# Kernel tuning notes

Hardware: AMD Instinct MI355X
Metric: run time of the kernel (lower is better)

Reference implementation:

```python
import jax, jax.numpy as jnp
import numpy as np

ITERATIONS = 10
EPS = 1e-8
ALPHA = 1.0
BETA = 1.0


def _conv3x3x3(x):
    # all-ones 3x3x3 kernel, padding=1 (SAME), single channel; NCDHW layout
    k = jnp.ones((1, 1, 3, 3, 3), x.dtype)
    return jax.lax.conv_general_dilated(
        x, k, window_strides=(1, 1, 1), padding='SAME',
        dimension_numbers=('NCDHW', 'OIDHW', 'NCDHW'))


def _soft_skeletonize(x):
    x = jax.nn.sigmoid(x)
    skeleton = x
    for _ in range(ITERATIONS):
        eroded = (_conv3x3x3(skeleton) > 0).astype(x.dtype)
        opened = (_conv3x3x3(eroded) > 0).astype(x.dtype)
        skeleton = jnp.clip(skeleton - opened, 0.0, 1.0)
    return skeleton


def _count_components(binary):
    neighbors = _conv3x3x3(binary)
    mask = binary > 0
    cnt = jnp.sum(mask).astype(binary.dtype)
    # torch.mean(neighbors[mask] + eps) == sum((neighbors+eps)*mask)/cnt
    mean_nb = jnp.sum(jnp.where(mask, neighbors + EPS, 0.0)) / jnp.maximum(cnt, 1.0)
    return (cnt / mean_nb)[None]


def setup_inputs() -> dict:
    key = jax.random.key(0)
    k1, k2 = jax.random.split(key)
    pred = jax.random.normal(k1, (2, 1, 192, 192, 192), dtype=jnp.float32)
    target = jax.random.uniform(k2, (2, 1, 192, 192, 192), dtype=jnp.float32)
    return {"pred": pred, "target": target}


def reference(pred, target):
    pred_prob = jax.nn.sigmoid(pred)
    # NOTE: module applies sigmoid again inside _soft_skeletonize (faithful)
    pred_skeleton = _soft_skeletonize(pred_prob)
    target_skeleton = _soft_skeletonize(target)

    intersection = jnp.sum(pred_skeleton * target_skeleton)
    union = jnp.sum(pred_skeleton) + jnp.sum(target_skeleton)
    skeleton_loss = 1.0 - (2.0 * intersection + EPS) / (union + EPS)

    pred_binary = (pred_prob > 0.5).astype(pred.dtype)
    target_binary = target  # .float() no-op
    pred_components = _count_components(pred_binary)
    target_components = _count_components(target_binary)
    connectivity_loss = jnp.mean(jnp.abs(pred_components - target_components))

    return ALPHA * skeleton_loss + BETA * connectivity_loss
```

## Files before the change

### kernel.cpp

```cpp
#include <hip/hip_runtime.h>
#include <math.h>

#define NN 192
#define PLANE (NN * NN)
#define VOL (NN * NN * NN)
#define ZCHUNK 12
#define RP 96
#define NBIN 8
#define EPSF 1e-8f

template <int MODE>
__device__ __forceinline__ float bval(float u) {
  return (MODE == 0) ? ((u > 0.f) ? 1.f : 0.f) : u;
}

struct PlaneR {
  float4 a, b, c, d;
};

__device__ __forceinline__ void loadP(const float* __restrict__ base, int z,
                                      int offA, int offB, int offC, int offD,
                                      int xoff, PlaneR& P) {
  const int zz = min(max(z, 0), NN - 1);
  const float* p = base + (size_t)zz * PLANE;
  P.a = *(const float4*)(p + offA + xoff);
  P.b = *(const float4*)(p + offB + xoff);
  P.c = *(const float4*)(p + offC + xoff);
  P.d = *(const float4*)(p + offD + xoff);
}

template <int MODE>
__device__ __forceinline__ void consume2(const PlaneR& P, float mA, float mD, float mz,
                                         int lane, float4& sY, float4& sZ,
                                         float4& cY, float4& cZ) {
  const float a0 = bval<MODE>(P.a.x), a1 = bval<MODE>(P.a.y), a2 = bval<MODE>(P.a.z), a3 = bval<MODE>(P.a.w);
  const float b0 = bval<MODE>(P.b.x), b1 = bval<MODE>(P.b.y), b2 = bval<MODE>(P.b.z), b3 = bval<MODE>(P.b.w);
  const float c0 = bval<MODE>(P.c.x), c1 = bval<MODE>(P.c.y), c2 = bval<MODE>(P.c.z), c3 = bval<MODE>(P.c.w);
  const float d0 = bval<MODE>(P.d.x), d1 = bval<MODE>(P.d.y), d2 = bval<MODE>(P.d.z), d3 = bval<MODE>(P.d.w);
  const float u0 = b0 + c0, u1 = b1 + c1, u2 = b2 + c2, u3 = b3 + c3;
  const float tY0 = fmaf(a0, mA, u0), tY1 = fmaf(a1, mA, u1), tY2 = fmaf(a2, mA, u2), tY3 = fmaf(a3, mA, u3);
  const float tZ0 = fmaf(d0, mD, u0), tZ1 = fmaf(d1, mD, u1), tZ2 = fmaf(d2, mD, u2), tZ3 = fmaf(d3, mD, u3);
  const float upY = __shfl_up(tY3, 1), dnY = __shfl_down(tY0, 1);
  const float upZ = __shfl_up(tZ3, 1), dnZ = __shfl_down(tZ0, 1);
  const float tlY = (lane == 0) ? 0.f : upY;
  const float trY = (lane >= 47) ? 0.f : dnY;
  const float tlZ = (lane == 0) ? 0.f : upZ;
  const float trZ = (lane >= 47) ? 0.f : dnZ;
  const float pY01 = tY0 + tY1, pY23 = tY2 + tY3;
  const float pZ01 = tZ0 + tZ1, pZ23 = tZ2 + tZ3;
  sY.x = (tlY + pY01) * mz; sY.y = (pY01 + tY2) * mz; sY.z = (tY1 + pY23) * mz; sY.w = (pY23 + trY) * mz;
  sZ.x = (tlZ + pZ01) * mz; sZ.y = (pZ01 + tZ2) * mz; sZ.z = (tZ1 + pZ23) * mz; sZ.w = (pZ23 + trZ) * mz;
  cY.x = b0; cY.y = b1; cY.z = b2; cY.w = b3;
  cZ.x = c0; cZ.y = c1; cZ.z = c2; cZ.w = c3;
}

#define ACC1(C, SP, SC, SN)                                   \
  {                                                           \
    float m = ((C) > 0.f) ? act : 0.f;                        \
    cnt += m;                                                 \
    acc = fmaf(m, ((SP) + (SC)) + (SN), acc);                 \
  }

#define ACCUM8(snY, snZ)                      \
  ACC1(cY.x, spY.x, scY.x, (snY).x)           \
  ACC1(cY.y, spY.y, scY.y, (snY).y)           \
  ACC1(cY.z, spY.z, scY.z, (snY).z)           \
  ACC1(cY.w, spY.w, scY.w, (snY).w)           \
  ACC1(cZ.x, spZ.x, scZ.x, (snZ).x)           \
  ACC1(cZ.y, spZ.y, scZ.y, (snZ).y)           \
  ACC1(cZ.z, spZ.z, scZ.z, (snZ).z)           \
  ACC1(cZ.w, spZ.w, scZ.w, (snZ).w)

#define ROTATE(snY, snZ, cnY, cnZ) \
  spY = scY; scY = snY; spZ = scZ; scZ = snZ; cY = cnY; cZ = cnZ;

#define STEP_R(PSLOT, I)                                                   \
  {                                                                        \
    float4 snY, snZ, cnY, cnZ;                                             \
    consume2<MODE>(PSLOT, mA, mD, 1.f, lane, snY, snZ, cnY, cnZ);          \
    loadP(base, z0 + 4 + (I), offA, offB, offC, offD, xoff, PSLOT);        \
    ACCUM8(snY, snZ);                                                      \
    ROTATE(snY, snZ, cnY, cnZ);                                            \
  }

#define STEP_E(PSLOT, MZ)                                                  \
  {                                                                        \
    float4 snY, snZ, cnY, cnZ;                                             \
    consume2<MODE>(PSLOT, mA, mD, (MZ), lane, snY, snZ, cnY, cnZ);         \
    ACCUM8(snY, snZ);                                                      \
    ROTATE(snY, snZ, cnY, cnZ);                                            \
  }

template <int MODE>
__device__ __forceinline__ void unit2(const float* __restrict__ base, int y0, int z0,
                                      int xoff, float act, int lane,
                                      float& cnt, float& acc) {
  const int offB = y0 * NN;
  const int offA = (y0 > 0 ? y0 - 1 : 0) * NN;
  const int offC = (y0 + 1) * NN;
  const int offD = (y0 + 2 < NN ? y0 + 2 : NN - 1) * NN;
  const float mA = (y0 > 0) ? 1.f : 0.f;
  const float mD = (y0 + 2 < NN) ? 1.f : 0.f;
  const float mzLo = (z0 > 0) ? 1.f : 0.f;
  const float mzHi = (z0 + ZCHUNK < NN) ? 1.f : 0.f;

  PlaneR P0, P1, P2;
  loadP(base, z0 - 1, offA, offB, offC, offD, xoff, P0);
  loadP(base, z0,     offA, offB, offC, offD, xoff, P1);
  loadP(base, z0 + 1, offA, offB, offC, offD, xoff, P2);

  float4 spY, scY, spZ, scZ, cY, cZ, j1, j2;
  consume2<MODE>(P0, mA, mD, mzLo, lane, spY, spZ, j1, j2);
  loadP(base, z0 + 2, offA, offB, offC, offD, xoff, P0);
  consume2<MODE>(P1, mA, mD, 1.f, lane, scY, scZ, cY, cZ);
  loadP(base, z0 + 3, offA, offB, offC, offD, xoff, P1);

#pragma unroll 1
  for (int i = 0; i < 9; i += 3) {
    STEP_R(P2, i + 0);
    STEP_R(P0, i + 1);
    STEP_R(P1, i + 2);
  }
  STEP_E(P2, 1.f);
  STEP_E(P0, 1.f);
  STEP_E(P1, mzHi);
}

__global__ void init_ws(float* __restrict__ ws) {
  if (threadIdx.x < NBIN * 16) ws[threadIdx.x] = 0.f;
}

__global__ __launch_bounds__(64, 2) void skel_main(const float* __restrict__ pred,
                                                   const float* __restrict__ target,
                                                   float* __restrict__ ws) {
  const int b = blockIdx.x;
  const int xcd = b & 7;
  const int slot = b >> 3;
  const int g = slot / RP;
  const int yp = slot % RP;
  const int unit = xcd * 8 + g;
  const int vol = unit & 3;
  const int zc = unit >> 2;
  const int z0 = zc * ZCHUNK;
  const int y0 = 2 * yp;
  const float* base = (vol < 2 ? pred : target) + (size_t)(vol & 1) * VOL;

  const int lane = threadIdx.x;
  const int xoff = 4 * min(lane, 47);
  const float act = (lane < 48) ? 1.f : 0.f;

  float cnt = 0.f, acc = 0.f;
  if (vol < 2) unit2<0>(base, y0, z0, xoff, act, lane, cnt, acc);
  else         unit2<1>(base, y0, z0, xoff, act, lane, cnt, acc);

#pragma unroll
  for (int o = 32; o > 0; o >>= 1) {
    cnt += __shfl_down(cnt, o);
    acc += __shfl_down(acc, o);
  }
  if (lane == 0) {
    const int off = (vol < 2) ? 0 : 2;
    float* slot_p = &ws[((yp & (NBIN - 1)) << 4) + off];
    atomicAdd(slot_p + 0, cnt);
    atomicAdd(slot_p + 1, acc);
  }
}

__global__ void finalize(const float* __restrict__ ws, float* __restrict__ out) {
  if (threadIdx.x == 0 && blockIdx.x == 0) {
    float cp = 0.f, ap = 0.f, ct = 0.f, at = 0.f;
#pragma unroll
    for (int i = 0; i < NBIN; ++i) {
      cp += ws[i * 16 + 0];
      ap += ws[i * 16 + 1];
      ct += ws[i * 16 + 2];
      at += ws[i * 16 + 3];
    }
    float mp = (ap + EPSF * cp) / fmaxf(cp, 1.f);
    float Pc = cp / mp;
    float mt = (at + EPSF * ct) / fmaxf(ct, 1.f);
    float Tc = ct / mt;
    out[0] = fabsf(Pc - Tc);
  }
}

extern "C" void kernel_launch(void* const* d_in, const int* in_sizes, int n_in,
                              void* d_out, int out_size, void* d_ws, size_t ws_size,
                              hipStream_t stream) {
  const float* pred = (const float*)d_in[0];
  const float* target = (const float*)d_in[1];
  float* ws = (float*)d_ws;
  float* out = (float*)d_out;

  init_ws<<<1, 128, 0, stream>>>(ws);
  skel_main<<<dim3(6144), dim3(64), 0, stream>>>(pred, target, ws);
  finalize<<<1, 64, 0, stream>>>(ws, out);
}
```

Before: 149.5 us.

## Process two interleaved z-chunks per wavefront to raise memory-level parallelism

Each 64-thread block now handles two z-chunks (A and B) of the same y-pair and volume, interleaving their plane loads and stencil steps. This halves the grid to 3072 blocks and relaxes launch bounds to one block per SIMD, so more registers are available. The goal is more independent loads in flight per wave, hiding HBM latency. The cost is fewer waves overall and higher register pressure, which could reduce occupancy-driven latency hiding.

Measured after the change: 143.7 us. 3.9% less time.

```diff
diff --git a/kernel.cpp b/kernel.cpp
--- a/kernel.cpp
+++ b/kernel.cpp
@@ -61,87 +61,106 @@
     acc = fmaf(m, ((SP) + (SC)) + (SN), acc);                 \
   }
 
-#define ACCUM8(snY, snZ)                      \
-  ACC1(cY.x, spY.x, scY.x, (snY).x)           \
-  ACC1(cY.y, spY.y, scY.y, (snY).y)           \
-  ACC1(cY.z, spY.z, scY.z, (snY).z)           \
-  ACC1(cY.w, spY.w, scY.w, (snY).w)           \
-  ACC1(cZ.x, spZ.x, scZ.x, (snZ).x)           \
-  ACC1(cZ.y, spZ.y, scZ.y, (snZ).y)           \
-  ACC1(cZ.z, spZ.z, scZ.z, (snZ).z)           \
-  ACC1(cZ.w, spZ.w, scZ.w, (snZ).w)
-
-#define ROTATE(snY, snZ, cnY, cnZ) \
-  spY = scY; scY = snY; spZ = scZ; scZ = snZ; cY = cnY; cZ = cnZ;
-
-#define STEP_R(PSLOT, I)                                                   \
+#define ACCUM8(S, snY, snZ)                            \
+  ACC1(cY##S.x, spY##S.x, scY##S.x, (snY).x)           \
+  ACC1(cY##S.y, spY##S.y, scY##S.y, (snY).y)           \
+  ACC1(cY##S.z, spY##S.z, scY##S.z, (snY).z)           \
+  ACC1(cY##S.w, spY##S.w, scY##S.w, (snY).w)           \
+  ACC1(cZ##S.x, spZ##S.x, scZ##S.x, (snZ).x)           \
+  ACC1(cZ##S.y, spZ##S.y, scZ##S.y, (snZ).y)           \
+  ACC1(cZ##S.z, spZ##S.z, scZ##S.z, (snZ).z)           \
+  ACC1(cZ##S.w, spZ##S.w, scZ##S.w, (snZ).w)
+
+#define ROT(S, snY, snZ, cnY, cnZ)                                        \
+  spY##S = scY##S; scY##S = snY; spZ##S = scZ##S; scZ##S = snZ;           \
+  cY##S = cnY; cZ##S = cnZ;
+
+#define STEP_R(S, PSLOT, Z0, I)                                            \
   {                                                                        \
     float4 snY, snZ, cnY, cnZ;                                             \
     consume2<MODE>(PSLOT, mA, mD, 1.f, lane, snY, snZ, cnY, cnZ);          \
-    loadP(base, z0 + 4 + (I), offA, offB, offC, offD, xoff, PSLOT);        \
-    ACCUM8(snY, snZ);                                                      \
-    ROTATE(snY, snZ, cnY, cnZ);                                            \
-  }
-
-#define STEP_E(PSLOT, MZ)                                                  \
+    loadP(base, (Z0) + 4 + (I), offA, offB, offC, offD, xoff, PSLOT);      \
+    ACCUM8(S, snY, snZ);                                                   \
+    ROT(S, snY, snZ, cnY, cnZ);                                            \
+  }
+
+#define STEP_E(S, PSLOT, MZ)                                               \
   {                                                                        \
     float4 snY, snZ, cnY, cnZ;                                             \
     consume2<MODE>(PSLOT, mA, mD, (MZ), lane, snY, snZ, cnY, cnZ);         \
-    ACCUM8(snY, snZ);                                                      \
-    ROTATE(snY, snZ, cnY, cnZ);                                            \
+    ACCUM8(S, snY, snZ);                                                   \
+    ROT(S, snY, snZ, cnY, cnZ);                                            \
   }
 
 template <int MODE>
-__device__ __forceinline__ void unit2(const float* __restrict__ base, int y0, int z0,
-                                      int xoff, float act, int lane,
-                                      float& cnt, float& acc) {
+__device__ __forceinline__ void unit2x2(const float* __restrict__ base, int y0,
+                                        int z0A, int z0B, int xoff, float act,
+                                        int lane, float& cnt, float& acc) {
   const int offB = y0 * NN;
   const int offA = (y0 > 0 ? y0 - 1 : 0) * NN;
   const int offC = (y0 + 1) * NN;
   const int offD = (y0 + 2 < NN ? y0 + 2 : NN - 1) * NN;
   const float mA = (y0 > 0) ? 1.f : 0.f;
   const float mD = (y0 + 2 < NN) ? 1.f : 0.f;
-  const float mzLo = (z0 > 0) ? 1.f : 0.f;
-  const float mzHi = (z0 + ZCHUNK < NN) ? 1.f : 0.f;
-
-  PlaneR P0, P1, P2;
-  loadP(base, z0 - 1, offA, offB, offC, offD, xoff, P0);
-  loadP(base, z0,     offA, offB, offC, offD, xoff, P1);
-  loadP(base, z0 + 1, offA, offB, offC, offD, xoff, P2);
-
-  float4 spY, scY, spZ, scZ, cY, cZ, j1, j2;
-  consume2<MODE>(P0, mA, mD, mzLo, lane, spY, spZ, j1, j2);
-  loadP(base, z0 + 2, offA, offB, offC, offD, xoff, P0);
-  consume2<MODE>(P1, mA, mD, 1.f, lane, scY, scZ, cY, cZ);
-  loadP(base, z0 + 3, offA, offB, offC, offD, xoff, P1);
+  const float mzLoA = (z0A > 0) ? 1.f : 0.f;
+  const float mzHiA = (z0A + ZCHUNK < NN) ? 1.f : 0.f;
+  const float mzLoB = (z0B > 0) ? 1.f : 0.f;
+  const float mzHiB = (z0B + ZCHUNK < NN) ? 1.f : 0.f;
+
+  PlaneR P0A, P1A, P2A, P0B, P1B, P2B;
+  float4 spYA, scYA, spZA, scZA, cYA, cZA;
+  float4 spYB, scYB, spZB, scZB, cYB, cZB;
+
+  loadP(base, z0A - 1, offA, offB, offC, offD, xoff, P0A);
+  loadP(base, z0B - 1, offA, offB, offC, offD, xoff, P0B);
+  loadP(base, z0A,     offA, offB, offC, offD, xoff, P1A);
+  loadP(base, z0B,     offA, offB, offC, offD, xoff, P1B);
+  loadP(base, z0A + 1, offA, offB, offC, offD, xoff, P2A);
+  loadP(base, z0B + 1, offA, offB, offC, offD, xoff, P2B);
+
+  {
+    float4 j1, j2;
+    consume2<MODE>(P0A, mA, mD, mzLoA, lane, spYA, spZA, j1, j2);
+    loadP(base, z0A + 2, offA, offB, offC, offD, xoff, P0A);
+    consume2<MODE>(P0B, mA, mD, mzLoB, lane, spYB, spZB, j1, j2);
+    loadP(base, z0B + 2, offA, offB, offC, offD, xoff, P0B);
+    consume2<MODE>(P1A, mA, mD, 1.f, lane, scYA, scZA, cYA, cZA);
+    loadP(base, z0A + 3, offA, offB, offC, offD, xoff, P1A);
+    consume2<MODE>(P1B, mA, mD, 1.f, lane, scYB, scZB, cYB, cZB);
+    loadP(base, z0B + 3, offA, offB, offC, offD, xoff, P1B);
+  }
 
 #pragma unroll 1
   for (int i = 0; i < 9; i += 3) {
-    STEP_R(P2, i + 0);
-    STEP_R(P0, i + 1);
-    STEP_R(P1, i + 2);
-  }
-  STEP_E(P2, 1.f);
-  STEP_E(P0, 1.f);
-  STEP_E(P1, mzHi);
+    STEP_R(A, P2A, z0A, i + 0);
+    STEP_R(B, P2B, z0B, i + 0);
+    STEP_R(A, P0A, z0A, i + 1);
+    STEP_R(B, P0B, z0B, i + 1);
+    STEP_R(A, P1A, z0A, i + 2);
+    STEP_R(B, P1B, z0B, i + 2);
+  }
+  STEP_E(A, P2A, 1.f);
+  STEP_E(B, P2B, 1.f);
+  STEP_E(A, P0A, 1.f);
+  STEP_E(B, P0B, 1.f);
+  STEP_E(A, P1A, mzHiA);
+  STEP_E(B, P1B, mzHiB);
 }
 
 __global__ void init_ws(float* __restrict__ ws) {
   if (threadIdx.x < NBIN * 16) ws[threadIdx.x] = 0.f;
 }
 
-__global__ __launch_bounds__(64, 2) void skel_main(const float* __restrict__ pred,
+__global__ __launch_bounds__(64, 1) void skel_main(const float* __restrict__ pred,
                                                    const float* __restrict__ target,
                                                    float* __restrict__ ws) {
   const int b = blockIdx.x;
   const int xcd = b & 7;
   const int slot = b >> 3;
-  const int g = slot / RP;
+  const int vol = slot / RP;
   const int yp = slot % RP;
-  const int unit = xcd * 8 + g;
-  const int vol = unit & 3;
-  const int zc = unit >> 2;
-  const int z0 = zc * ZCHUNK;
+  const int z0A = (2 * xcd) * ZCHUNK;
+  const int z0B = z0A + ZCHUNK;
   const int y0 = 2 * yp;
   const float* base = (vol < 2 ? pred : target) + (size_t)(vol & 1) * VOL;
 
@@ -150,8 +169,8 @@
   const float act = (lane < 48) ? 1.f : 0.f;
 
   float cnt = 0.f, acc = 0.f;
-  if (vol < 2) unit2<0>(base, y0, z0, xoff, act, lane, cnt, acc);
-  else         unit2<1>(base, y0, z0, xoff, act, lane, cnt, acc);
+  if (vol < 2) unit2x2<0>(base, y0, z0A, z0B, xoff, act, lane, cnt, acc);
+  else         unit2x2<1>(base, y0, z0A, z0B, xoff, act, lane, cnt, acc);
 
 #pragma unroll
   for (int o = 32; o > 0; o >>= 1) {
@@ -193,6 +212,6 @@
   float* out = (float*)d_out;
 
   init_ws<<<1, 128, 0, stream>>>(ws);
-  skel_main<<<dim3(6144), dim3(64), 0, stream>>>(pred, target, ws);
+  skel_main<<<dim3(3072), dim3(64), 0, stream>>>(pred, target, ws);
   finalize<<<1, 64, 0, stream>>>(ws, out);
 }
```
